# Optimization experiments

Hardware: AMD Instinct MI355X
Metric: run time of the kernel (lower is better)

The kernel has to match this reference:

```python
import jax, jax.numpy as jnp
import numpy as np

B, N, NFEAT, NHID, NHEADS, NCLASS, K1 = 4, 2048, 256, 64, 4, 32, 256
ALPHA = 0.2      # leaky relu slope
NEG = -9e15      # mask value used by the torch impl


def setup_inputs() -> dict:
    key = jax.random.key(0)
    ks = jax.random.split(key, 16)
    s = 0.05
    return {
        "x": jax.random.normal(ks[0], (B, N, NFEAT), jnp.float32),
        "adj": jax.random.randint(ks[1], (B, N, N), 0, 2).astype(jnp.int32),
        "one_hop_idcs": jax.random.randint(ks[2], (B, K1), 0, N),
        # multi-head GAT layer params (stacked over heads)
        "W": jax.random.normal(ks[3], (NHEADS, NFEAT, NHID), jnp.float32) * s,
        "a1": jax.random.normal(ks[4], (NHEADS, NHID), jnp.float32) * s,  # a[:nhid]
        "a2": jax.random.normal(ks[5], (NHEADS, NHID), jnp.float32) * s,  # a[nhid:]
        # output GAT layer params
        "Wo": jax.random.normal(ks[6], (NHEADS * NHID, NCLASS), jnp.float32) * s,
        "ao1": jax.random.normal(ks[7], (NCLASS,), jnp.float32) * s,
        "ao2": jax.random.normal(ks[8], (NCLASS,), jnp.float32) * s,
        # classifier: Linear(32, nclass) -> PReLU(nclass) -> Linear(nclass, 2)
        "W1": jax.random.normal(ks[9], (NCLASS, NCLASS), jnp.float32) * s,
        "b1": jnp.zeros((NCLASS,), jnp.float32),
        "prelu_w": jnp.full((NCLASS,), 0.25, jnp.float32),
        "W2": jax.random.normal(ks[10], (NCLASS, 2), jnp.float32) * s,
        "b2": jnp.zeros((2,), jnp.float32),
    }


def _gat_heads(x, W, a1, a2, adj):
    """Dense multi-head GAT. e_ij = leakyrelu(a^T [Wh_i || Wh_j]) computed
    as broadcast of two rank-1 projections (no [N,N,2d] concat tensor)."""
    Wh = jnp.einsum('bnf,hfd->bhnd', x, W)                 # [B,H,N,d]
    f1 = jnp.einsum('bhnd,hd->bhn', Wh, a1)                # src term
    f2 = jnp.einsum('bhnd,hd->bhn', Wh, a2)                # dst term
    e = jax.nn.leaky_relu(f1[:, :, :, None] + f2[:, :, None, :], ALPHA)
    e = jnp.where(adj[:, None, :, :] > 0, e, NEG)
    attn = jax.nn.softmax(e, axis=-1)                      # [B,H,N,N]
    h = jnp.einsum('bhnm,bhmd->bhnd', attn, Wh)            # [B,H,N,d]
    h = jax.nn.elu(h)                                      # concat=True -> elu
    # concat heads: [B,N,H*d]
    return h.transpose(0, 2, 1, 3).reshape(x.shape[0], x.shape[1], -1)


def _gat_out(x, Wo, ao1, ao2, adj):
    Wh = x @ Wo                                            # [B,N,nclass]
    f1 = Wh @ ao1
    f2 = Wh @ ao2
    e = jax.nn.leaky_relu(f1[:, :, None] + f2[:, None, :], ALPHA)
    e = jnp.where(adj > 0, e, NEG)
    attn = jax.nn.softmax(e, axis=-1)
    return attn @ Wh                                       # concat=False -> no elu here


def reference(x, adj, one_hop_idcs, W, a1, a2, Wo, ao1, ao2,
              W1, b1, prelu_w, W2, b2):
    h = _gat_heads(x, W, a1, a2, adj)          # [B,N,H*nhid]
    h = jax.nn.elu(_gat_out(h, Wo, ao1, ao2, adj))  # [B,N,nclass]
    # vectorized per-batch gather (replaces python loop over b)
    ef = jnp.take_along_axis(h, one_hop_idcs[:, :, None], axis=1)  # [B,K1,nclass]
    ef = ef.reshape(-1, h.shape[-1])
    y = ef @ W1 + b1
    y = jnp.where(y > 0, y, prelu_w * y)       # PReLU(nclass)
    return y @ W2 + b2                         # [B*K1, 2]
```

## Files before the change

### kernel.cpp

```cpp
#include <hip/hip_runtime.h>
#include <hip/hip_bf16.h>
#include <stdint.h>
#include <math.h>

#define BB 4
#define NN 2048
#define NFEAT 256
#define NHID 64
#define NHEADS 4
#define NCLASS 32
#define KK1 256
#define ALPHA 0.2f
#define LOG2E 1.4426950408889634f

typedef _Float16 f16x8 __attribute__((ext_vector_type(8)));
typedef _Float16 f16x4 __attribute__((ext_vector_type(4)));
typedef _Float16 h16x2 __attribute__((ext_vector_type(2)));
typedef float f32x4 __attribute__((ext_vector_type(4)));

__device__ __forceinline__ f16x8 ld8(const _Float16* p){
  f16x8 r;
  *(f16x4*)&r = *(const f16x4*)p;
  *((f16x4*)&r + 1) = *(const f16x4*)(p + 4);
  return r;
}

__device__ __forceinline__ h16x2 pk2(float a, float b){
  auto v = __builtin_amdgcn_cvt_pkrtz(a, b);
  h16x2 r;
  __builtin_memcpy(&r, &v, sizeof(r));
  return r;
}

__global__ void __launch_bounds__(256) pack_adj(const int* __restrict__ adj,
                                                unsigned long long* __restrict__ bits,
                                                int* __restrict__ cnt){
  __shared__ int csum[4];
  int row = blockIdx.x;
  const int* arow = adj + (size_t)row * NN;
  int lane = threadIdx.x & 63, wv = threadIdx.x >> 6;
  int c = 0;
  #pragma unroll
  for (int it=0; it<NN/256; ++it){
    int j = it*256 + threadIdx.x;
    unsigned long long m = __ballot(arow[j] > 0);
    if (lane==0){ bits[(size_t)row*(NN/64) + it*4 + wv] = m; c += __popcll(m); }
  }
  if (lane==0) csum[wv] = c;
  __syncthreads();
  if (threadIdx.x==0) cnt[row] = csum[0]+csum[1]+csum[2]+csum[3];
}

__global__ void __launch_bounds__(256) wh_proj2(const float* __restrict__ x,
        const float* __restrict__ W, const float* __restrict__ a1, const float* __restrict__ a2,
        _Float16* __restrict__ whT, float* __restrict__ f1l, float* __restrict__ f2l){
  __shared__ __align__(16) float xs[64*65];
  __shared__ float red1[4][64];
  __shared__ float red2[4][64];
  int bh = blockIdx.x >> 5;
  int i0 = (blockIdx.x & 31) * 64;
  int b = bh >> 2, h = bh & 3;
  int tid = threadIdx.x;
  int lane = tid & 63;
  int dbase = __builtin_amdgcn_readfirstlane(tid >> 6) * 16;
  float acc[16];
  #pragma unroll
  for (int dd=0; dd<16; ++dd) acc[dd] = 0.f;
  for (int kc=0; kc<4; ++kc){
    int kb = kc*64;
    __syncthreads();
    #pragma unroll
    for (int t=0; t<4; ++t){
      int row = t*16 + (tid>>4);
      int f4 = (tid&15)*4;
      float4 v = *(const float4*)(x + ((size_t)(b*NN + i0 + row))*NFEAT + kb + f4);
      xs[row*65 + f4 + 0] = v.x;
      xs[row*65 + f4 + 1] = v.y;
      xs[row*65 + f4 + 2] = v.z;
      xs[row*65 + f4 + 3] = v.w;
    }
    __syncthreads();
    const float* Wb = W + (size_t)h*NFEAT*NHID + (size_t)kb*NHID + dbase;
    #pragma unroll 4
    for (int f=0; f<64; ++f){
      float xv = xs[lane*65 + f];
      const float* wr = Wb + f*NHID;
      #pragma unroll
      for (int dd=0; dd<16; ++dd) acc[dd] = fmaf(xv, wr[dd], acc[dd]);
    }
  }
  float p1 = 0.f, p2 = 0.f;
  #pragma unroll
  for (int dd=0; dd<16; ++dd){
    int d = dbase + dd;
    whT[((size_t)bh*NHID + d)*NN + i0 + lane] = (_Float16)acc[dd];
    p1 = fmaf(acc[dd], a1[h*NHID + d], p1);
    p2 = fmaf(acc[dd], a2[h*NHID + d], p2);
  }
  int wv = tid >> 6;
  red1[wv][lane] = p1;
  red2[wv][lane] = p2;
  __syncthreads();
  if (tid < 64){
    float s1 = red1[0][tid]+red1[1][tid]+red1[2][tid]+red1[3][tid];
    float s2 = red2[0][tid]+red2[1][tid]+red2[2][tid]+red2[3][tid];
    f1l[(size_t)bh*NN + i0 + tid] = s1 * LOG2E;
    f2l[(size_t)bh*NN + i0 + tid] = s2 * LOG2E;
  }
}

__global__ void __launch_bounds__(256) attn_l1(
        const unsigned long long* __restrict__ bits,
        const _Float16* __restrict__ whT,
        const float* __restrict__ f1l, const float* __restrict__ f2l,
        const int* __restrict__ cnt_in,
        float* __restrict__ dst){
  const int PITCH = 136;
  __shared__ __align__(16) _Float16 whs[64*PITCH];
  __shared__ float ils[4][16];
  int tile = blockIdx.x & 31;
  int bh = blockIdx.x >> 5;
  int b = bh >> 2, h = bh & 3;
  int i0 = tile*64;
  int tid = threadIdx.x;
  int lane = tid & 63, w = tid >> 6;
  int q = lane >> 4, col = lane & 15;
  int mrow = i0 + w*16 + col;
  float f1r = f1l[(size_t)bh*NN + mrow];
  bool cz = (cnt_in[b*NN + mrow] == 0);
  const unsigned int* mr = (const unsigned int*)(bits + ((size_t)(b*NN + mrow))*(NN/64));
  const float* f2p = f2l + (size_t)bh*NN;
  const _Float16* whg = whT + (size_t)bh*NHID*NN;
  int sd = tid >> 2, sq = tid & 3;
  const _Float16* sg = whg + (size_t)sd*NN + sq*32;
  _Float16* sl = whs + sd*PITCH + sq*32;
  float lacc = 0.f;
  f32x4 acc[4];
  #pragma unroll
  for (int nt=0; nt<4; ++nt) acc[nt] = f32x4{0.f,0.f,0.f,0.f};

  for (int it=0; it<16; ++it){
    __syncthreads();
    {
      uint4 t0 = *(const uint4*)(sg + it*128);
      uint4 t1 = *(const uint4*)(sg + it*128 + 8);
      uint4 t2 = *(const uint4*)(sg + it*128 + 16);
      uint4 t3 = *(const uint4*)(sg + it*128 + 24);
      *(uint4*)(sl)      = t0;
      *(uint4*)(sl + 8)  = t1;
      *(uint4*)(sl + 16) = t2;
      *(uint4*)(sl + 24) = t3;
    }
    uint4 mw4 = *(const uint4*)(mr + it*4);
    __syncthreads();
    #pragma unroll
    for (int ks=0; ks<4; ++ks){
      unsigned int mw = ((const unsigned int*)&mw4)[ks];
      int j8 = it*128 + ks*32 + q*8;
      float4 fa = *(const float4*)(f2p + j8);
      float4 fb = *(const float4*)(f2p + j8 + 4);
      float fv[8] = {fa.x,fa.y,fa.z,fa.w, fb.x,fb.y,fb.z,fb.w};
      union { f16x8 v; h16x2 h[4]; } ua;
      #pragma unroll
      for (int p=0; p<4; ++p){
        unsigned sh = q*8 + 2*p;
        float s0 = f1r + fv[2*p];
        float s1 = f1r + fv[2*p+1];
        s0 = ((mw>>sh)&1u)     ? s0 : -1e5f;
        s1 = ((mw>>(sh+1))&1u) ? s1 : -1e5f;
        float w0 = __builtin_amdgcn_exp2f(fmaxf(s0, ALPHA*s0));
        float w1 = __builtin_amdgcn_exp2f(fmaxf(s1, ALPHA*s1));
        w0 = cz ? 1.f : w0;
        w1 = cz ? 1.f : w1;
        lacc += w0 + w1;
        ua.h[p] = pk2(w0, w1);
      }
      #pragma unroll
      for (int nt=0; nt<4; ++nt){
        f16x8 bv = ld8(&whs[(nt*16 + col)*PITCH + ks*32 + q*8]);
        acc[nt] = __builtin_amdgcn_mfma_f32_16x16x32_f16(ua.v, bv, acc[nt], 0, 0, 0);
      }
    }
  }
  lacc += __shfl_xor(lacc, 16, 64);
  lacc += __shfl_xor(lacc, 32, 64);
  if (q == 0) ils[w][col] = 1.0f / lacc;
  __syncthreads();
  #pragma unroll
  for (int reg=0; reg<4; ++reg){
    int ir = q*4 + reg;
    float ilv = ils[w][ir];
    float* dp = dst + ((size_t)(b*NN + i0 + w*16 + ir))*(NHEADS*NHID) + h*NHID + col;
    #pragma unroll
    for (int nt=0; nt<4; ++nt){
      float v = acc[nt][reg] * ilv;
      v = v > 0.f ? v : expm1f(v);
      dp[nt*16] = v;
    }
  }
}

__global__ void __launch_bounds__(256) out_proj2(const float* __restrict__ h1,
        const float* __restrict__ Wo, const float* __restrict__ ao1, const float* __restrict__ ao2,
        _Float16* __restrict__ whT2, float* __restrict__ f1ol, float* __restrict__ f2ol){
  __shared__ __align__(16) float xs[64*65];
  __shared__ float red1[4][64];
  __shared__ float red2[4][64];
  int b = blockIdx.x >> 5;
  int i0 = (blockIdx.x & 31) * 64;
  int tid = threadIdx.x;
  int lane = tid & 63;
  int dbase = __builtin_amdgcn_readfirstlane(tid >> 6) * 8;
  float acc[8];
  #pragma unroll
  for (int dd=0; dd<8; ++dd) acc[dd] = 0.f;
  for (int kc=0; kc<4; ++kc){
    int kb = kc*64;
    __syncthreads();
    #pragma unroll
    for (int t=0; t<4; ++t){
      int row = t*16 + (tid>>4);
      int f4 = (tid&15)*4;
      float4 v = *(const float4*)(h1 + ((size_t)(b*NN + i0 + row))*256 + kb + f4);
      xs[row*65 + f4 + 0] = v.x;
      xs[row*65 + f4 + 1] = v.y;
      xs[row*65 + f4 + 2] = v.z;
      xs[row*65 + f4 + 3] = v.w;
    }
    __syncthreads();
    #pragma unroll 4
    for (int f=0; f<64; ++f){
      float xv = xs[lane*65 + f];
      const float* wr = Wo + (size_t)(kb+f)*NCLASS + dbase;
      #pragma unroll
      for (int dd=0; dd<8; ++dd) acc[dd] = fmaf(xv, wr[dd], acc[dd]);
    }
  }
  float p1 = 0.f, p2 = 0.f;
  #pragma unroll
  for (int dd=0; dd<8; ++dd){
    int d = dbase + dd;
    whT2[((size_t)b*NCLASS + d)*NN + i0 + lane] = (_Float16)acc[dd];
    p1 = fmaf(acc[dd], ao1[d], p1);
    p2 = fmaf(acc[dd], ao2[d], p2);
  }
  int wv = tid >> 6;
  red1[wv][lane] = p1;
  red2[wv][lane] = p2;
  __syncthreads();
  if (tid < 64){
    float s1 = red1[0][tid]+red1[1][tid]+red1[2][tid]+red1[3][tid];
    float s2 = red2[0][tid]+red2[1][tid]+red2[2][tid]+red2[3][tid];
    f1ol[(size_t)b*NN + i0 + tid] = s1 * LOG2E;
    f2ol[(size_t)b*NN + i0 + tid] = s2 * LOG2E;
  }
}

__global__ void __launch_bounds__(256) attn_l2(
        const unsigned long long* __restrict__ bits,
        const _Float16* __restrict__ whT2,
        const float* __restrict__ f1ol, const float* __restrict__ f2ol,
        const int* __restrict__ cnt_in, const int* __restrict__ oh,
        float* __restrict__ pc, float* __restrict__ pl){
  const int JC = 128, PITCH = 132;
  __shared__ __align__(16) _Float16 whs[32*PITCH];
  __shared__ __align__(16) _Float16 wts[32*PITCH];
  int blk = blockIdx.x;
  int js = blk & 7, kt = (blk>>3) & 7, b = blk >> 6;
  int tid = threadIdx.x;
  int lane = tid & 63, wv = tid >> 6;
  int q = lane >> 4, col = lane & 15;
  int r = tid >> 3, jg = (tid & 7) * 16;
  int row_i = oh[b*KK1 + kt*32 + r];
  float f1r = f1ol[b*NN + row_i];
  bool czr = (cnt_in[b*NN + row_i] == 0);
  const unsigned short* mrow = (const unsigned short*)(bits + ((size_t)(b*NN + row_i))*(NN/64));
  const float* f2p = f2ol + (size_t)b*NN;
  const _Float16* whg = whT2 + (size_t)b*NCLASS*NN;
  float lacc = 0.f;
  f32x4 c0 = {0.f,0.f,0.f,0.f};
  int mt = wv & 1, nt = wv >> 1;
  for (int ii=0; ii<2; ++ii){
    int it = js*2 + ii;
    __syncthreads();
    #pragma unroll
    for (int dd=0; dd<2; ++dd){
      int d = (tid>>4) + dd*16;
      int j8 = (tid&15)*8;
      uint4 v = *(const uint4*)(whg + (size_t)d*NN + it*JC + j8);
      uint2* w2 = (uint2*)&whs[d*PITCH + j8];
      w2[0] = uint2{v.x, v.y};
      w2[1] = uint2{v.z, v.w};
    }
    {
      unsigned int m16 = mrow[it*8 + (tid&7)];
      const float* fp = f2p + it*JC + jg;
      float4 fa = *(const float4*)(fp);
      float4 fb = *(const float4*)(fp+4);
      float4 fc = *(const float4*)(fp+8);
      float4 fd = *(const float4*)(fp+12);
      float fv[16] = {fa.x,fa.y,fa.z,fa.w, fb.x,fb.y,fb.z,fb.w,
                      fc.x,fc.y,fc.z,fc.w, fd.x,fd.y,fd.z,fd.w};
      h16x2 wp[8];
      #pragma unroll
      for (int p=0; p<8; ++p){
        float s0 = f1r + fv[2*p];
        float s1 = f1r + fv[2*p+1];
        s0 = (m16 & (1u<<(2*p)))   ? s0 : -1e5f;
        s1 = (m16 & (1u<<(2*p+1))) ? s1 : -1e5f;
        float e0 = fmaxf(s0, ALPHA*s0);
        float e1 = fmaxf(s1, ALPHA*s1);
        float w0 = __builtin_amdgcn_exp2f(e0);
        float w1 = __builtin_amdgcn_exp2f(e1);
        lacc += w0 + w1;
        wp[p] = pk2(w0, w1);
      }
      if (__builtin_expect(czr, 0)){
        h16x2 one2 = {(_Float16)1.f, (_Float16)1.f};
        #pragma unroll
        for (int p=0; p<8; ++p) wp[p] = one2;
        lacc += 16.f;
      }
      uint2* wdst = (uint2*)&wts[r*PITCH + jg];
      const uint2* wsrc = (const uint2*)&wp[0];
      wdst[0]=wsrc[0]; wdst[1]=wsrc[1]; wdst[2]=wsrc[2]; wdst[3]=wsrc[3];
    }
    __syncthreads();
    #pragma unroll
    for (int ks=0; ks<4; ++ks){
      int kb = ks*32 + q*8;
      f16x8 a0 = ld8(&wts[(mt*16+col)*PITCH + kb]);
      f16x8 bv = ld8(&whs[(nt*16+col)*PITCH + kb]);
      c0 = __builtin_amdgcn_mfma_f32_16x16x32_f16(a0, bv, c0, 0, 0, 0);
    }
  }
  lacc += __shfl_xor(lacc, 1, 64);
  lacc += __shfl_xor(lacc, 2, 64);
  lacc += __shfl_xor(lacc, 4, 64);
  if ((tid & 7) == 0) pl[blk*32 + r] = lacc;
  int dloc = nt*16 + col;
  #pragma unroll
  for (int reg=0; reg<4; ++reg){
    int ir = mt*16 + q*4 + reg;
    pc[(size_t)blk*1024 + ir*32 + dloc] = c0[reg];
  }
}

__global__ void __launch_bounds__(256) classify2(const float* __restrict__ pc,
        const float* __restrict__ pl,
        const float* __restrict__ W1, const float* __restrict__ b1,
        const float* __restrict__ pw, const float* __restrict__ W2, const float* __restrict__ b2,
        float* __restrict__ out){
  __shared__ float efs[4][32];
  int wv = threadIdx.x >> 6;
  int lane = threadIdx.x & 63;
  int row = blockIdx.x*4 + wv;
  int b = row >> 8, k = row & 255;
  int kt = k >> 5, r = k & 31;
  int base = (b*8 + kt)*8;
  if (lane < 32){
    float s = 0.f, l = 0.f;
    #pragma unroll
    for (int js=0; js<8; ++js){
      s += pc[(size_t)(base+js)*1024 + r*32 + lane];
      l += pl[(base+js)*32 + r];
    }
    float v = s / l;
    v = v > 0.f ? v : expm1f(v);
    efs[wv][lane] = v;
  }
  __syncthreads();
  const float* ef = efs[wv];
  int c = lane & 31;
  float y = b1[c];
  #pragma unroll 8
  for (int kk=0; kk<32; ++kk) y += ef[kk] * W1[kk*32 + c];
  y = y > 0.f ? y : pw[c]*y;
  float o0 = y * W2[c*2+0];
  float o1 = y * W2[c*2+1];
  #pragma unroll
  for (int o=16;o>0;o>>=1){ o0 += __shfl_xor(o0,o,64); o1 += __shfl_xor(o1,o,64); }
  if (lane==0){ out[row*2+0] = o0 + b2[0]; out[row*2+1] = o1 + b2[1]; }
}

extern "C" void kernel_launch(void* const* d_in, const int* in_sizes, int n_in,
                              void* d_out, int out_size, void* d_ws, size_t ws_size,
                              hipStream_t stream) {
  const float* x    = (const float*)d_in[0];
  const int*   adj  = (const int*)  d_in[1];
  const int*   oh   = (const int*)  d_in[2];
  const float* W    = (const float*)d_in[3];
  const float* a1   = (const float*)d_in[4];
  const float* a2   = (const float*)d_in[5];
  const float* Wo   = (const float*)d_in[6];
  const float* ao1  = (const float*)d_in[7];
  const float* ao2  = (const float*)d_in[8];
  const float* W1   = (const float*)d_in[9];
  const float* b1   = (const float*)d_in[10];
  const float* pw   = (const float*)d_in[11];
  const float* W2   = (const float*)d_in[12];
  const float* b2   = (const float*)d_in[13];
  float* out = (float*)d_out;

  char* base = (char*)d_ws;
  size_t off = 0;
  auto alloc = [&](size_t bytes)->char*{
    char* p = base + off;
    off = (off + bytes + 255) & ~(size_t)255;
    return p;
  };
  unsigned long long* adjbits = (unsigned long long*)alloc((size_t)BB*NN*(NN/64)*8);
  int*   cnt1 = (int*)  alloc((size_t)BB*NN*4);
  _Float16* WhT  = (_Float16*)alloc((size_t)BB*NHEADS*NHID*NN*2);
  float* f1l  = (float*)alloc((size_t)BB*NHEADS*NN*4);
  float* f2l  = (float*)alloc((size_t)BB*NHEADS*NN*4);
  float* h1   = (float*)alloc((size_t)BB*NN*(NHEADS*NHID)*4);
  _Float16* WhT2 = (_Float16*)alloc((size_t)BB*NCLASS*NN*2);
  float* f1ol = (float*)alloc((size_t)BB*NN*4);
  float* f2ol = (float*)alloc((size_t)BB*NN*4);
  float* pc   = (float*)alloc((size_t)256*1024*4);
  float* pl   = (float*)alloc((size_t)256*32*4);

  pack_adj<<<BB*NN, 256, 0, stream>>>(adj, adjbits, cnt1);
  wh_proj2<<<BB*NHEADS*(NN/64), 256, 0, stream>>>(x, W, a1, a2, WhT, f1l, f2l);
  attn_l1<<<BB*NHEADS*(NN/64), 256, 0, stream>>>(adjbits, WhT, f1l, f2l, cnt1, h1);
  out_proj2<<<BB*(NN/64), 256, 0, stream>>>(h1, Wo, ao1, ao2, WhT2, f1ol, f2ol);
  attn_l2<<<BB*8*8, 256, 0, stream>>>(adjbits, WhT2, f1ol, f2ol, cnt1, oh, pc, pl);
  classify2<<<(BB*KK1)/4, 256, 0, stream>>>(pc, pl, W1, b1, pw, W2, b2, out);
}
```

Baseline: 235.0 us.

## Factor attention exponentials into per-node terms and split-K the layer-1 attention

```diff
diff --git a/kernel.cpp b/kernel.cpp
--- a/kernel.cpp
+++ b/kernel.cpp
@@ -14,14 +14,12 @@
 #define LOG2E 1.4426950408889634f
 
 typedef _Float16 f16x8 __attribute__((ext_vector_type(8)));
-typedef _Float16 f16x4 __attribute__((ext_vector_type(4)));
 typedef _Float16 h16x2 __attribute__((ext_vector_type(2)));
 typedef float f32x4 __attribute__((ext_vector_type(4)));
 
-__device__ __forceinline__ f16x8 ld8(const _Float16* p){
+__device__ __forceinline__ f16x8 ldb128(const _Float16* p){
   f16x8 r;
-  *(f16x4*)&r = *(const f16x4*)p;
-  *((f16x4*)&r + 1) = *(const f16x4*)(p + 4);
+  *(uint4*)&r = *(const uint4*)p;
   return r;
 }
 
@@ -53,7 +51,9 @@
 
 __global__ void __launch_bounds__(256) wh_proj2(const float* __restrict__ x,
         const float* __restrict__ W, const float* __restrict__ a1, const float* __restrict__ a2,
-        _Float16* __restrict__ whT, float* __restrict__ f1l, float* __restrict__ f2l){
+        _Float16* __restrict__ whT,
+        float* __restrict__ ex1, float* __restrict__ gx1,
+        float* __restrict__ ex2, float* __restrict__ gx2){
   __shared__ __align__(16) float xs[64*65];
   __shared__ float red1[4][64];
   __shared__ float red2[4][64];
@@ -102,38 +102,44 @@
   red2[wv][lane] = p2;
   __syncthreads();
   if (tid < 64){
-    float s1 = red1[0][tid]+red1[1][tid]+red1[2][tid]+red1[3][tid];
-    float s2 = red2[0][tid]+red2[1][tid]+red2[2][tid]+red2[3][tid];
-    f1l[(size_t)bh*NN + i0 + tid] = s1 * LOG2E;
-    f2l[(size_t)bh*NN + i0 + tid] = s2 * LOG2E;
-  }
-}
-
-__global__ void __launch_bounds__(256) attn_l1(
+    float s1 = (red1[0][tid]+red1[1][tid]+red1[2][tid]+red1[3][tid]) * LOG2E;
+    float s2 = (red2[0][tid]+red2[1][tid]+red2[2][tid]+red2[3][tid]) * LOG2E;
+    size_t o = (size_t)bh*NN + i0 + tid;
+    ex1[o] = __builtin_amdgcn_exp2f(s1);
+    gx1[o] = __builtin_amdgcn_exp2f(ALPHA*s1);
+    ex2[o] = __builtin_amdgcn_exp2f(s2);
+    gx2[o] = __builtin_amdgcn_exp2f(ALPHA*s2);
+  }
+}
+
+__global__ void __launch_bounds__(256, 8) attn_l1(
         const unsigned long long* __restrict__ bits,
         const _Float16* __restrict__ whT,
-        const float* __restrict__ f1l, const float* __restrict__ f2l,
+        const float* __restrict__ ex1, const float* __restrict__ gx1,
+        const float* __restrict__ ex2, const float* __restrict__ gx2,
         const int* __restrict__ cnt_in,
         float* __restrict__ dst){
   const int PITCH = 136;
   __shared__ __align__(16) _Float16 whs[64*PITCH];
-  __shared__ float ils[4][16];
-  int tile = blockIdx.x & 31;
-  int bh = blockIdx.x >> 5;
+  __shared__ float lred[4][16];
+  int tile = blockIdx.x & 127;
+  int bh = blockIdx.x >> 7;
   int b = bh >> 2, h = bh & 3;
-  int i0 = tile*64;
+  int i0 = tile*16;
   int tid = threadIdx.x;
   int lane = tid & 63, w = tid >> 6;
   int q = lane >> 4, col = lane & 15;
-  int mrow = i0 + w*16 + col;
-  float f1r = f1l[(size_t)bh*NN + mrow];
-  bool cz = (cnt_in[b*NN + mrow] == 0);
+  int mrow = i0 + col;
+  size_t ro = (size_t)bh*NN + mrow;
+  float E1 = ex1[ro], G1 = gx1[ro];
+  float fz = (cnt_in[b*NN + mrow] == 0) ? 1.f : 0.f;
   const unsigned int* mr = (const unsigned int*)(bits + ((size_t)(b*NN + mrow))*(NN/64));
-  const float* f2p = f2l + (size_t)bh*NN;
+  const float* e2p = ex2 + (size_t)bh*NN;
+  const float* g2p = gx2 + (size_t)bh*NN;
   const _Float16* whg = whT + (size_t)bh*NHID*NN;
-  int sd = tid >> 2, sq = tid & 3;
-  const _Float16* sg = whg + (size_t)sd*NN + sq*32;
-  _Float16* sl = whs + sd*PITCH + sq*32;
+  int sd = tid >> 2, ss = tid & 3;
+  const _Float16* sg = whg + (size_t)sd*NN + ss*512;
+  _Float16* sl = whs + sd*PITCH + ss*32;
   float lacc = 0.f;
   f32x4 acc[4];
   #pragma unroll
@@ -142,67 +148,69 @@
   for (int it=0; it<16; ++it){
     __syncthreads();
     {
-      uint4 t0 = *(const uint4*)(sg + it*128);
-      uint4 t1 = *(const uint4*)(sg + it*128 + 8);
-      uint4 t2 = *(const uint4*)(sg + it*128 + 16);
-      uint4 t3 = *(const uint4*)(sg + it*128 + 24);
-      *(uint4*)(sl)      = t0;
-      *(uint4*)(sl + 8)  = t1;
-      *(uint4*)(sl + 16) = t2;
-      *(uint4*)(sl + 24) = t3;
-    }
-    uint4 mw4 = *(const uint4*)(mr + it*4);
-    __syncthreads();
-    #pragma unroll
-    for (int ks=0; ks<4; ++ks){
-      unsigned int mw = ((const unsigned int*)&mw4)[ks];
-      int j8 = it*128 + ks*32 + q*8;
-      float4 fa = *(const float4*)(f2p + j8);
-      float4 fb = *(const float4*)(f2p + j8 + 4);
-      float fv[8] = {fa.x,fa.y,fa.z,fa.w, fb.x,fb.y,fb.z,fb.w};
-      union { f16x8 v; h16x2 h[4]; } ua;
-      #pragma unroll
-      for (int p=0; p<4; ++p){
-        unsigned sh = q*8 + 2*p;
-        float s0 = f1r + fv[2*p];
-        float s1 = f1r + fv[2*p+1];
-        s0 = ((mw>>sh)&1u)     ? s0 : -1e5f;
-        s1 = ((mw>>(sh+1))&1u) ? s1 : -1e5f;
-        float w0 = __builtin_amdgcn_exp2f(fmaxf(s0, ALPHA*s0));
-        float w1 = __builtin_amdgcn_exp2f(fmaxf(s1, ALPHA*s1));
-        w0 = cz ? 1.f : w0;
-        w1 = cz ? 1.f : w1;
-        lacc += w0 + w1;
-        ua.h[p] = pk2(w0, w1);
-      }
-      #pragma unroll
-      for (int nt=0; nt<4; ++nt){
-        f16x8 bv = ld8(&whs[(nt*16 + col)*PITCH + ks*32 + q*8]);
-        acc[nt] = __builtin_amdgcn_mfma_f32_16x16x32_f16(ua.v, bv, acc[nt], 0, 0, 0);
-      }
+      const uint4* g4 = (const uint4*)(sg + it*32);
+      uint4 t0 = g4[0], t1 = g4[1], t2 = g4[2], t3 = g4[3];
+      uint4* l4 = (uint4*)sl;
+      l4[0]=t0; l4[1]=t1; l4[2]=t2; l4[3]=t3;
+    }
+    unsigned int mw = mr[w*16 + it] >> (q*8);
+    int jb = w*512 + it*32 + q*8;
+    float4 ea = *(const float4*)(e2p + jb);
+    float4 eb = *(const float4*)(e2p + jb + 4);
+    float4 ga = *(const float4*)(g2p + jb);
+    float4 gb = *(const float4*)(g2p + jb + 4);
+    __syncthreads();
+    float ev[8] = {ea.x,ea.y,ea.z,ea.w, eb.x,eb.y,eb.z,eb.w};
+    float gv[8] = {ga.x,ga.y,ga.z,ga.w, gb.x,gb.y,gb.z,gb.w};
+    union { f16x8 v; h16x2 hh[4]; } ua;
+    #pragma unroll
+    for (int p=0; p<4; ++p){
+      float w0 = ((mw>>(2*p))&1u)   ? fmaxf(E1*ev[2*p],   G1*gv[2*p])   : fz;
+      float w1 = ((mw>>(2*p+1))&1u) ? fmaxf(E1*ev[2*p+1], G1*gv[2*p+1]) : fz;
+      lacc += w0 + w1;
+      ua.hh[p] = pk2(w0, w1);
+    }
+    #pragma unroll
+    for (int nt=0; nt<4; ++nt){
+      f16x8 bv = ldb128(&whs[(nt*16 + col)*PITCH + w*32 + q*8]);
+      acc[nt] = __builtin_amdgcn_mfma_f32_16x16x32_f16(ua.v, bv, acc[nt], 0, 0, 0);
     }
   }
   lacc += __shfl_xor(lacc, 16, 64);
   lacc += __shfl_xor(lacc, 32, 64);
-  if (q == 0) ils[w][col] = 1.0f / lacc;
-  __syncthreads();
-  #pragma unroll
-  for (int reg=0; reg<4; ++reg){
-    int ir = q*4 + reg;
-    float ilv = ils[w][ir];
-    float* dp = dst + ((size_t)(b*NN + i0 + w*16 + ir))*(NHEADS*NHID) + h*NHID + col;
-    #pragma unroll
-    for (int nt=0; nt<4; ++nt){
-      float v = acc[nt][reg] * ilv;
-      v = v > 0.f ? v : expm1f(v);
-      dp[nt*16] = v;
-    }
-  }
+  if (q == 0) lred[w][col] = lacc;
+  __syncthreads();
+  float* cred = (float*)whs;
+  #pragma unroll
+  for (int nt=0; nt<4; ++nt)
+    #pragma unroll
+    for (int reg=0; reg<4; ++reg)
+      cred[(w*16 + q*4 + reg)*68 + nt*16 + col] = acc[nt][reg];
+  __syncthreads();
+  int row = tid >> 4, dg = (tid & 15) * 4;
+  float l = lred[0][row] + lred[1][row] + lred[2][row] + lred[3][row];
+  float il = 1.0f / l;
+  float4 s = {0,0,0,0};
+  #pragma unroll
+  for (int ww=0; ww<4; ++ww){
+    float4 v = *(const float4*)&cred[(ww*16 + row)*68 + dg];
+    s.x+=v.x; s.y+=v.y; s.z+=v.z; s.w+=v.w;
+  }
+  float ov[4] = {s.x,s.y,s.z,s.w};
+  #pragma unroll
+  for (int dd=0; dd<4; ++dd){
+    float v = ov[dd]*il;
+    ov[dd] = v > 0.f ? v : expm1f(v);
+  }
+  *(float4*)(dst + ((size_t)(b*NN + i0 + row))*(NHEADS*NHID) + h*NHID + dg)
+      = float4{ov[0],ov[1],ov[2],ov[3]};
 }
 
 __global__ void __launch_bounds__(256) out_proj2(const float* __restrict__ h1,
         const float* __restrict__ Wo, const float* __restrict__ ao1, const float* __restrict__ ao2,
-        _Float16* __restrict__ whT2, float* __restrict__ f1ol, float* __restrict__ f2ol){
+        _Float16* __restrict__ whT2,
+        float* __restrict__ eo1, float* __restrict__ go1,
+        float* __restrict__ eo2, float* __restrict__ go2){
   __shared__ __align__(16) float xs[64*65];
   __shared__ float red1[4][64];
   __shared__ float red2[4][64];
@@ -249,20 +257,24 @@
   red2[wv][lane] = p2;
   __syncthreads();
   if (tid < 64){
-    float s1 = red1[0][tid]+red1[1][tid]+red1[2][tid]+red1[3][tid];
-    float s2 = red2[0][tid]+red2[1][tid]+red2[2][tid]+red2[3][tid];
-    f1ol[(size_t)b*NN + i0 + tid] = s1 * LOG2E;
-    f2ol[(size_t)b*NN + i0 + tid] = s2 * LOG2E;
+    float s1 = (red1[0][tid]+red1[1][tid]+red1[2][tid]+red1[3][tid]) * LOG2E;
+    float s2 = (red2[0][tid]+red2[1][tid]+red2[2][tid]+red2[3][tid]) * LOG2E;
+    size_t o = (size_t)b*NN + i0 + tid;
+    eo1[o] = __builtin_amdgcn_exp2f(s1);
+    go1[o] = __builtin_amdgcn_exp2f(ALPHA*s1);
+    eo2[o] = __builtin_amdgcn_exp2f(s2);
+    go2[o] = __builtin_amdgcn_exp2f(ALPHA*s2);
   }
 }
 
 __global__ void __launch_bounds__(256) attn_l2(
         const unsigned long long* __restrict__ bits,
         const _Float16* __restrict__ whT2,
-        const float* __restrict__ f1ol, const float* __restrict__ f2ol,
+        const float* __restrict__ eo1, const float* __restrict__ go1,
+        const float* __restrict__ eo2, const float* __restrict__ go2,
         const int* __restrict__ cnt_in, const int* __restrict__ oh,
         float* __restrict__ pc, float* __restrict__ pl){
-  const int JC = 128, PITCH = 132;
+  const int JC = 128, PITCH = 136;
   __shared__ __align__(16) _Float16 whs[32*PITCH];
   __shared__ __align__(16) _Float16 wts[32*PITCH];
   int blk = blockIdx.x;
@@ -272,10 +284,11 @@
   int q = lane >> 4, col = lane & 15;
   int r = tid >> 3, jg = (tid & 7) * 16;
   int row_i = oh[b*KK1 + kt*32 + r];
-  float f1r = f1ol[b*NN + row_i];
-  bool czr = (cnt_in[b*NN + row_i] == 0);
+  float E1 = eo1[b*NN + row_i], G1 = go1[b*NN + row_i];
+  float fz = (cnt_in[b*NN + row_i] == 0) ? 1.f : 0.f;
   const unsigned short* mrow = (const unsigned short*)(bits + ((size_t)(b*NN + row_i))*(NN/64));
-  const float* f2p = f2ol + (size_t)b*NN;
+  const float* e2p = eo2 + (size_t)b*NN;
+  const float* g2p = go2 + (size_t)b*NN;
   const _Float16* whg = whT2 + (size_t)b*NCLASS*NN;
   float lacc = 0.f;
   f32x4 c0 = {0.f,0.f,0.f,0.f};
@@ -287,50 +300,36 @@
     for (int dd=0; dd<2; ++dd){
       int d = (tid>>4) + dd*16;
       int j8 = (tid&15)*8;
-      uint4 v = *(const uint4*)(whg + (size_t)d*NN + it*JC + j8);
-      uint2* w2 = (uint2*)&whs[d*PITCH + j8];
-      w2[0] = uint2{v.x, v.y};
-      w2[1] = uint2{v.z, v.w};
+      *(uint4*)&whs[d*PITCH + j8] = *(const uint4*)(whg + (size_t)d*NN + it*JC + j8);
     }
     {
       unsigned int m16 = mrow[it*8 + (tid&7)];
-      const float* fp = f2p + it*JC + jg;
-      float4 fa = *(const float4*)(fp);
-      float4 fb = *(const float4*)(fp+4);
-      float4 fc = *(const float4*)(fp+8);
-      float4 fd = *(const float4*)(fp+12);
-      float fv[16] = {fa.x,fa.y,fa.z,fa.w, fb.x,fb.y,fb.z,fb.w,
-                      fc.x,fc.y,fc.z,fc.w, fd.x,fd.y,fd.z,fd.w};
-      h16x2 wp[8];
+      const float* ep = e2p + it*JC + jg;
+      const float* gp = g2p + it*JC + jg;
+      float ev[16], gv[16];
+      #pragma unroll
+      for (int t4=0; t4<4; ++t4){
+        *(float4*)&ev[t4*4] = *(const float4*)(ep + t4*4);
+        *(float4*)&gv[t4*4] = *(const float4*)(gp + t4*4);
+      }
+      union { h16x2 hh[8]; uint4 u4[2]; } wp;
       #pragma unroll
       for (int p=0; p<8; ++p){
-        float s0 = f1r + fv[2*p];
-        float s1 = f1r + fv[2*p+1];
-        s0 = (m16 & (1u<<(2*p)))   ? s0 : -1e5f;
-        s1 = (m16 & (1u<<(2*p+1))) ? s1 : -1e5f;
-        float e0 = fmaxf(s0, ALPHA*s0);
-        float e1 = fmaxf(s1, ALPHA*s1);
-        float w0 = __builtin_amdgcn_exp2f(e0);
-        float w1 = __builtin_amdgcn_exp2f(e1);
+        float w0 = (m16 & (1u<<(2*p)))   ? fmaxf(E1*ev[2*p],   G1*gv[2*p])   : fz;
+        float w1 = (m16 & (1u<<(2*p+1))) ? fmaxf(E1*ev[2*p+1], G1*gv[2*p+1]) : fz;
         lacc += w0 + w1;
-        wp[p] = pk2(w0, w1);
+        wp.hh[p] = pk2(w0, w1);
       }
-      if (__builtin_expect(czr, 0)){
-        h16x2 one2 = {(_Float16)1.f, (_Float16)1.f};
-        #pragma unroll
-        for (int p=0; p<8; ++p) wp[p] = one2;
-        lacc += 16.f;
-      }
-      uint2* wdst = (uint2*)&wts[r*PITCH + jg];
-      const uint2* wsrc = (const uint2*)&wp[0];
-      wdst[0]=wsrc[0]; wdst[1]=wsrc[1]; wdst[2]=wsrc[2]; wdst[3]=wsrc[3];
+      uint4* wdst = (uint4*)&wts[r*PITCH + jg];
+      wdst[0] = wp.u4[0];
+      wdst[1] = wp.u4[1];
     }
     __syncthreads();
     #pragma unroll
     for (int ks=0; ks<4; ++ks){
       int kb = ks*32 + q*8;
-      f16x8 a0 = ld8(&wts[(mt*16+col)*PITCH + kb]);
-      f16x8 bv = ld8(&whs[(nt*16+col)*PITCH + kb]);
+      f16x8 a0 = ldb128(&wts[(mt*16+col)*PITCH + kb]);
+      f16x8 bv = ldb128(&whs[(nt*16+col)*PITCH + kb]);
       c0 = __builtin_amdgcn_mfma_f32_16x16x32_f16(a0, bv, c0, 0, 0, 0);
     }
   }
@@ -412,19 +411,23 @@
   unsigned long long* adjbits = (unsigned long long*)alloc((size_t)BB*NN*(NN/64)*8);
   int*   cnt1 = (int*)  alloc((size_t)BB*NN*4);
   _Float16* WhT  = (_Float16*)alloc((size_t)BB*NHEADS*NHID*NN*2);
-  float* f1l  = (float*)alloc((size_t)BB*NHEADS*NN*4);
-  float* f2l  = (float*)alloc((size_t)BB*NHEADS*NN*4);
+  float* ex1  = (float*)alloc((size_t)BB*NHEADS*NN*4);
+  float* gx1  = (float*)alloc((size_t)BB*NHEADS*NN*4);
+  float* ex2  = (float*)alloc((size_t)BB*NHEADS*NN*4);
+  float* gx2  = (float*)alloc((size_t)BB*NHEADS*NN*4);
   float* h1   = (float*)alloc((size_t)BB*NN*(NHEADS*NHID)*4);
   _Float16* WhT2 = (_Float16*)alloc((size_t)BB*NCLASS*NN*2);
-  float* f1ol = (float*)alloc((size_t)BB*NN*4);
-  float* f2ol = (float*)alloc((size_t)BB*NN*4);
+  float* eo1  = (float*)alloc((size_t)BB*NN*4);
+  float* go1  = (float*)alloc((size_t)BB*NN*4);
+  float* eo2  = (float*)alloc((size_t)BB*NN*4);
+  float* go2  = (float*)alloc((size_t)BB*NN*4);
   float* pc   = (float*)alloc((size_t)256*1024*4);
   float* pl   = (float*)alloc((size_t)256*32*4);
 
   pack_adj<<<BB*NN, 256, 0, stream>>>(adj, adjbits, cnt1);
-  wh_proj2<<<BB*NHEADS*(NN/64), 256, 0, stream>>>(x, W, a1, a2, WhT, f1l, f2l);
-  attn_l1<<<BB*NHEADS*(NN/64), 256, 0, stream>>>(adjbits, WhT, f1l, f2l, cnt1, h1);
-  out_proj2<<<BB*(NN/64), 256, 0, stream>>>(h1, Wo, ao1, ao2, WhT2, f1ol, f2ol);
-  attn_l2<<<BB*8*8, 256, 0, stream>>>(adjbits, WhT2, f1ol, f2ol, cnt1, oh, pc, pl);
+  wh_proj2<<<BB*NHEADS*(NN/64), 256, 0, stream>>>(x, W, a1, a2, WhT, ex1, gx1, ex2, gx2);
+  attn_l1<<<BB*NHEADS*(NN/16), 256, 0, stream>>>(adjbits, WhT, ex1, gx1, ex2, gx2, cnt1, h1);
+  out_proj2<<<BB*(NN/64), 256, 0, stream>>>(h1, Wo, ao1, ao2, WhT2, eo1, go1, eo2, go2);
+  attn_l2<<<BB*8*8, 256, 0, stream>>>(adjbits, WhT2, eo1, go1, eo2, go2, cnt1, oh, pc, pl);
   classify2<<<(BB*KK1)/4, 256, 0, stream>>>(pc, pl, W1, b1, pw, W2, b2, out);
 }
```

Result: slower. 264.7 us (+12.6%).
